# Kernel optimization log

Hardware: AMD Instinct MI355X
Metric: run time of the kernel (lower is better)

Reference implementation:

```python
import jax, jax.numpy as jnp
import numpy as np

B, H, O, T = 4096, 256, 128, 200

def setup_inputs() -> dict:
    key = jax.random.key(0)
    ks = jax.random.split(key, 8)
    s = 1.0 / np.sqrt(H)
    return {
        "C": jax.random.normal(ks[0], (B, H), dtype=jnp.float32),
        "t": jax.random.randint(ks[1], (B,), 0, T),
        "mask": jnp.ones((B, T), dtype=jnp.float32),
        "W_ih": jax.random.uniform(ks[2], (4 * H, H), jnp.float32, -s, s),
        "W_hh": jax.random.uniform(ks[3], (4 * H, H), jnp.float32, -s, s),
        "b_ih": jax.random.uniform(ks[4], (4 * H,), jnp.float32, -s, s),
        "b_hh": jax.random.uniform(ks[5], (4 * H,), jnp.float32, -s, s),
        "W_lin": jax.random.uniform(ks[6], (O, H), jnp.float32, -s, s),
        "b_lin": jax.random.uniform(ks[7], (O,), jnp.float32, -s, s),
    }

def reference(C, t, mask, W_ih, W_hh, b_ih, b_hh, W_lin, b_lin):
    # Input projection is constant across time (same C fed every step).
    x_proj = C @ W_ih.T + b_ih + b_hh  # [B, 4H]
    h0 = jnp.zeros((C.shape[0], W_hh.shape[1]), dtype=C.dtype)
    c0 = jnp.zeros_like(h0)

    def step(carry, _):
        h, c = carry
        gates = x_proj + h @ W_hh.T          # [B, 4H], torch gate order i,f,g,o
        i, f, g, o = jnp.split(gates, 4, axis=-1)
        i = jax.nn.sigmoid(i)
        f = jax.nn.sigmoid(f)
        g = jnp.tanh(g)
        o = jax.nn.sigmoid(o)
        c = f * c + i * g
        h = o * jnp.tanh(c)
        y = h @ W_lin.T + b_lin              # [B, O]
        return (h, c), y

    _, ys = jax.lax.scan(step, (h0, c0), xs=None, length=T)
    return ys  # [T, B, O]
```

## Files before the change

### kernel.cpp

```cpp
#include <hip/hip_runtime.h>


#define B_SZ 4096
#define H_SZ 256
#define O_SZ 128
#define T_SZ 200
#define SW   2032.0f
#define SG   (1.0f/(127.0f*2032.0f))

typedef __bf16 b16x8 __attribute__((ext_vector_type(8)));
typedef float f32x4 __attribute__((ext_vector_type(4)));
typedef int   i32x4 __attribute__((ext_vector_type(4)));
typedef unsigned short u16x8 __attribute__((ext_vector_type(8)));

typedef __attribute__((address_space(1))) const void gas_void;
typedef __attribute__((address_space(3))) void las_void;

__device__ __forceinline__ unsigned short f2bf(float x){
  unsigned u = __builtin_bit_cast(unsigned, x);
  u += 0x7FFFu + ((u >> 16) & 1u);
  return (unsigned short)(u >> 16);
}
__device__ __forceinline__ float bf2f(unsigned short h){
  unsigned u = ((unsigned)h) << 16;
  return __builtin_bit_cast(float, u);
}
__device__ __forceinline__ float fsig(float x){
  float t = __builtin_amdgcn_exp2f(-1.4426950408889634f * x);
  return __builtin_amdgcn_rcpf(1.0f + t);
}
__device__ __forceinline__ float ftanh(float x){
  x = fminf(fmaxf(x, -15.0f), 15.0f);
  float e = __builtin_amdgcn_exp2f(2.8853900817779268f * x);
  return (e - 1.0f) * __builtin_amdgcn_rcpf(e + 1.0f);
}
__device__ __forceinline__ f32x4 mfma16(b16x8 a, b16x8 b, f32x4 c){
  return __builtin_amdgcn_mfma_f32_16x16x32_bf16(a, b, c, 0, 0, 0);
}
__device__ __forceinline__ i32x4 mfma_i8(i32x4 a, i32x4 b, i32x4 c){
  return __builtin_amdgcn_mfma_i32_16x16x64_i8(a, b, c, 0, 0, 0);
}

__global__ void lstm_setup(const float* __restrict__ Wih, const float* __restrict__ Whh,
                           const float* __restrict__ Wlin, const float* __restrict__ bih,
                           const float* __restrict__ bhh, const float* __restrict__ C,
                           unsigned short* __restrict__ pWih, signed char* __restrict__ qWhh,
                           signed char* __restrict__ qWlin, float* __restrict__ bias,
                           unsigned short* __restrict__ Chi, unsigned short* __restrict__ Clo)
{
  const int nW  = 262144;
  const int nQ  = 262144;
  const int nL  = 32768;
  const int nB  = 1024;
  const int nC  = 1048576;
  long i = (long)blockIdx.x * blockDim.x + threadIdx.x;
  if (i < nW){
    int d = (int)i;
    int j = d & 7, l = (d >> 3) & 63, nt = (d >> 9) & 63, kk = (d >> 15) & 7;
    int src = (nt * 16 + (l & 15)) * H_SZ + kk * 32 + (l >> 4) * 8 + j;
    pWih[d] = f2bf(Wih[src]);
  } else if (i < nW + nQ){
    int d = (int)(i - nW);
    int j = d & 15, l = (d >> 4) & 63, kk = (d >> 10) & 3, nt = d >> 12;
    int n = nt * 16 + (l & 15), k = kk * 64 + (l >> 4) * 16 + j;
    qWhh[d] = (signed char)(int)rintf(Whh[n * H_SZ + k] * SW);
  } else if (i < nW + nQ + nL){
    int d = (int)(i - nW - nQ);
    int j = d & 15, l = (d >> 4) & 63, kk = (d >> 10) & 3, nt = d >> 12;
    int n = nt * 16 + (l & 15), k = kk * 64 + (l >> 4) * 16 + j;
    qWlin[d] = (signed char)(int)rintf(Wlin[n * H_SZ + k] * SW);
  } else if (i < nW + nQ + nL + nB){
    int d = (int)(i - nW - nQ - nL);
    bias[d] = bih[d] + bhh[d];
  } else if (i < nW + nQ + nL + nB + nC){
    int d = (int)(i - nW - nQ - nL - nB);
    float c = C[d];
    unsigned short hi = f2bf(c);
    Chi[d] = hi;
    Clo[d] = f2bf(c - bf2f(hi));
  }
}

__device__ __forceinline__ b16x8 ldsA(const unsigned short* hb, int row, int kbyte){
  int off = row * 512 + (kbyte ^ ((row & 15) << 4));
  return *(const b16x8*)((const char*)hb + off);
}
__device__ __forceinline__ b16x8 ldB2(const unsigned short* __restrict__ p, int ntile, int kk, int l){
  return *(const b16x8*)(p + (((kk * 64 + ntile) << 6) + l) * 8);
}
__device__ __forceinline__ i32x4 ldh(const char* h8, int row, int kbase){
  int off = row * 256 + (kbase ^ ((row & 15) << 4));
  return *(const i32x4*)(h8 + off);
}

__launch_bounds__(1024, 1)
__global__ void lstm_main(const unsigned short* __restrict__ pWih,
                          const signed char* __restrict__ qWhh,
                          const signed char* __restrict__ qWlin,
                          const float* __restrict__ bias,
                          const unsigned short* __restrict__ Chi,
                          const unsigned short* __restrict__ Clo,
                          const float* __restrict__ blin,
                          float* __restrict__ out)
{
  __shared__ char smem[4096 + 32768];
  char* h8 = smem;
  char* wlin = smem + 4096;
  unsigned short* ctile = (unsigned short*)(smem + 4096);

  const int tid = threadIdx.x;
  const int w = tid >> 6, l = tid & 63;
  const int lm = l & 15, lg = l >> 4;
  const int B0 = blockIdx.x * 16;

  f32x4 accf[4];
  const f32x4 zf = {0.f,0.f,0.f,0.f};
  #pragma unroll
  for (int g = 0; g < 4; g++) accf[g] = zf;

  for (int pass = 0; pass < 2; pass++){
    const unsigned short* Csrc = pass ? Clo : Chi;
    __syncthreads();
    if (tid < 512){
      int r = tid >> 5, c0 = (tid & 31) * 8;
      u16x8 v = *(const u16x8*)(Csrc + (long)(B0 + r) * H_SZ + c0);
      *(u16x8*)((char*)ctile + r * 512 + ((c0 * 2) ^ (r << 4))) = v;
    }
    __syncthreads();
    #pragma unroll
    for (int kk = 0; kk < 8; kk++){
      b16x8 a0 = ldsA(ctile, lm, kk * 64 + lg * 16);
      #pragma unroll
      for (int g = 0; g < 4; g++){
        b16x8 b = ldB2(pWih, g * 16 + w, kk, l);
        accf[g] = mfma16(a0, b, accf[g]);
      }
    }
  }
  f32x4 xpf[4];
  #pragma unroll
  for (int g = 0; g < 4; g++){
    float bv = bias[(g * 16 + w) * 16 + lm];
    #pragma unroll
    for (int r = 0; r < 4; r++) xpf[g][r] = accf[g][r] + bv;
  }
  __syncthreads();

  i32x4 bW[4][4];
  #pragma unroll
  for (int g = 0; g < 4; g++)
    #pragma unroll
    for (int kk = 0; kk < 4; kk++)
      bW[g][kk] = *(const i32x4*)(qWhh + ((g * 16 + w) * 4 + kk) * 1024 + l * 16);
  #pragma unroll
  for (int f = 0; f < 2; f++)
    __builtin_amdgcn_global_load_lds(
        (gas_void*)(qWlin + (w * 2 + f) * 1024 + l * 16),
        (las_void*)(wlin + (w * 2 + f) * 1024 + l * 16), 16, 0, 0);
  float bl = (w < 8) ? blin[w * 16 + lm] : 0.f;

  float cst[4];
  #pragma unroll
  for (int r = 0; r < 4; r++) cst[r] = 0.f;

  *(unsigned*)(h8 + tid * 4) = 0u;
  asm volatile("s_waitcnt vmcnt(0) lgkmcnt(0)" ::: "memory");
  __builtin_amdgcn_s_barrier();

  for (int t = 0; t < T_SZ; t++){
    i32x4 acci[4];
    const i32x4 zi = {0,0,0,0};
    #pragma unroll
    for (int g = 0; g < 4; g++) acci[g] = zi;

    #pragma unroll
    for (int kk = 0; kk < 4; kk++){
      i32x4 a = ldh(h8, lm, kk * 64 + lg * 16);
      #pragma unroll
      for (int g = 0; g < 4; g++)
        acci[g] = mfma_i8(a, bW[g][kk], acci[g]);
    }
    asm volatile("s_waitcnt lgkmcnt(0)" ::: "memory");
    __builtin_amdgcn_s_barrier();

    #pragma unroll
    for (int r = 0; r < 4; r++){
      float iv = fsig (SG * (float)acci[0][r] + xpf[0][r]);
      float fv = fsig (SG * (float)acci[1][r] + xpf[1][r]);
      float gv = ftanh(SG * (float)acci[2][r] + xpf[2][r]);
      float ov = fsig (SG * (float)acci[3][r] + xpf[3][r]);
      float cn = fv * cst[r] + iv * gv;
      cst[r] = cn;
      float hv = ov * ftanh(cn);
      int row = lg * 4 + r;
      int col = w * 16 + lm;
      h8[row * 256 + (col ^ (row << 4))] = (signed char)(int)rintf(hv * 127.0f);
    }
    asm volatile("s_waitcnt lgkmcnt(0)" ::: "memory");
    __builtin_amdgcn_s_barrier();

    if (w < 8){
      i32x4 ya = zi;
      #pragma unroll
      for (int kk = 0; kk < 4; kk++){
        i32x4 a  = ldh(h8, lm, kk * 64 + lg * 16);
        i32x4 bb = *(const i32x4*)(wlin + (w * 4 + kk) * 1024 + l * 16);
        ya = mfma_i8(a, bb, ya);
      }
      float* op = out + (long)t * (B_SZ * O_SZ) + (long)B0 * O_SZ;
      #pragma unroll
      for (int r = 0; r < 4; r++){
        int row = lg * 4 + r;
        __builtin_nontemporal_store(SG * (float)ya[r] + bl, op + row * O_SZ + w * 16 + lm);
      }
    }
  }
}

extern "C" void kernel_launch(void* const* d_in, const int* in_sizes, int n_in,
                              void* d_out, int out_size, void* d_ws, size_t ws_size,
                              hipStream_t stream)
{
  const float* C    = (const float*)d_in[0];
  const float* Wih  = (const float*)d_in[3];
  const float* Whh  = (const float*)d_in[4];
  const float* bih  = (const float*)d_in[5];
  const float* bhh  = (const float*)d_in[6];
  const float* Wlin = (const float*)d_in[7];
  const float* blin = (const float*)d_in[8];
  float* out = (float*)d_out;

  char* ws = (char*)d_ws;
  unsigned short* pWih = (unsigned short*)(ws);
  signed char*    qWhh = (signed char*)(ws + 524288);
  signed char*    qWlin= (signed char*)(ws + 786432);
  float*          bias = (float*)(ws + 819200);
  unsigned short* Chi  = (unsigned short*)(ws + 823296);
  unsigned short* Clo  = (unsigned short*)(ws + 2920448);

  int total = 262144 + 262144 + 32768 + 1024 + 1048576;
  lstm_setup<<<dim3((total + 255) / 256), dim3(256), 0, stream>>>(
      Wih, Whh, Wlin, bih, bhh, C, pWih, qWhh, qWlin, bias, Chi, Clo);
  lstm_main<<<dim3(256), dim3(1024), 0, stream>>>(
      pWih, qWhh, qWlin, bias, Chi, Clo, blin, out);
}
```

Before: 410.1 us.

## Double-buffer hidden state and defer output projection to drop a barrier

The int8 hidden state in LDS is double-buffered, so each step reads h from one buffer and writes the next into the other. This removes one of the two per-step barriers. The output projection for step t-1 now reuses the h fragments already loaded for the recurrent matmul, with a final epilogue for the last step. Gate nonlinearities are also folded so the exp2 scale constants are premultiplied into x_proj and the accumulator scale, and tanh is expressed via a sigmoid-style rcp. Costs are extra LDS and the loss of the tanh clamp, which could overflow exp2 for large arguments (rcp of inf gives 0, so the result stays finite).

```diff
diff --git a/kernel.cpp b/kernel.cpp
--- a/kernel.cpp
+++ b/kernel.cpp
@@ -7,6 +7,8 @@
 #define T_SZ 200
 #define SW   2032.0f
 #define SG   (1.0f/(127.0f*2032.0f))
+#define KC   (-1.4426950408889634f)
+#define K2C  (-2.8853900817779268f)
 
 typedef __bf16 b16x8 __attribute__((ext_vector_type(8)));
 typedef float f32x4 __attribute__((ext_vector_type(4)));
@@ -25,15 +27,8 @@
   unsigned u = ((unsigned)h) << 16;
   return __builtin_bit_cast(float, u);
 }
-__device__ __forceinline__ float fsig(float x){
-  float t = __builtin_amdgcn_exp2f(-1.4426950408889634f * x);
-  return __builtin_amdgcn_rcpf(1.0f + t);
-}
-__device__ __forceinline__ float ftanh(float x){
-  x = fminf(fmaxf(x, -15.0f), 15.0f);
-  float e = __builtin_amdgcn_exp2f(2.8853900817779268f * x);
-  return (e - 1.0f) * __builtin_amdgcn_rcpf(e + 1.0f);
-}
+__device__ __forceinline__ float fexp2(float x){ return __builtin_amdgcn_exp2f(x); }
+__device__ __forceinline__ float frcp(float x){ return __builtin_amdgcn_rcpf(x); }
 __device__ __forceinline__ f32x4 mfma16(b16x8 a, b16x8 b, f32x4 c){
   return __builtin_amdgcn_mfma_f32_16x16x32_bf16(a, b, c, 0, 0, 0);
 }
@@ -103,10 +98,10 @@
                           const float* __restrict__ blin,
                           float* __restrict__ out)
 {
-  __shared__ char smem[4096 + 32768];
+  __shared__ char smem[8192 + 32768];
   char* h8 = smem;
-  char* wlin = smem + 4096;
-  unsigned short* ctile = (unsigned short*)(smem + 4096);
+  char* wlin = smem + 8192;
+  unsigned short* ctile = (unsigned short*)(smem + 8192);
 
   const int tid = threadIdx.x;
   const int w = tid >> 6, l = tid & 63;
@@ -137,12 +132,13 @@
       }
     }
   }
-  f32x4 xpf[4];
+  f32x4 xs[4];
   #pragma unroll
   for (int g = 0; g < 4; g++){
     float bv = bias[(g * 16 + w) * 16 + lm];
-    #pragma unroll
-    for (int r = 0; r < 4; r++) xpf[g][r] = accf[g][r] + bv;
+    float sc = (g == 2) ? K2C : KC;
+    #pragma unroll
+    for (int r = 0; r < 4; r++) xs[g][r] = sc * (accf[g][r] + bv);
   }
   __syncthreads();
 
@@ -163,57 +159,84 @@
   #pragma unroll
   for (int r = 0; r < 4; r++) cst[r] = 0.f;
 
-  *(unsigned*)(h8 + tid * 4) = 0u;
+  *(unsigned long long*)(h8 + tid * 8) = 0ull;
   asm volatile("s_waitcnt vmcnt(0) lgkmcnt(0)" ::: "memory");
   __builtin_amdgcn_s_barrier();
 
+  const float KnS  = KC  * SG;
+  const float K2S  = K2C * SG;
+  const i32x4 zi = {0,0,0,0};
+
   for (int t = 0; t < T_SZ; t++){
+    const char* hrd = h8 + (t & 1) * 4096;
+    char*       hwr = h8 + ((t + 1) & 1) * 4096;
+
+    i32x4 a[4];
+    #pragma unroll
+    for (int kk = 0; kk < 4; kk++) a[kk] = ldh(hrd, lm, kk * 64 + lg * 16);
+
     i32x4 acci[4];
-    const i32x4 zi = {0,0,0,0};
     #pragma unroll
     for (int g = 0; g < 4; g++) acci[g] = zi;
-
-    #pragma unroll
-    for (int kk = 0; kk < 4; kk++){
-      i32x4 a = ldh(h8, lm, kk * 64 + lg * 16);
+    #pragma unroll
+    for (int kk = 0; kk < 4; kk++)
       #pragma unroll
       for (int g = 0; g < 4; g++)
-        acci[g] = mfma_i8(a, bW[g][kk], acci[g]);
-    }
-    asm volatile("s_waitcnt lgkmcnt(0)" ::: "memory");
-    __builtin_amdgcn_s_barrier();
-
-    #pragma unroll
-    for (int r = 0; r < 4; r++){
-      float iv = fsig (SG * (float)acci[0][r] + xpf[0][r]);
-      float fv = fsig (SG * (float)acci[1][r] + xpf[1][r]);
-      float gv = ftanh(SG * (float)acci[2][r] + xpf[2][r]);
-      float ov = fsig (SG * (float)acci[3][r] + xpf[3][r]);
-      float cn = fv * cst[r] + iv * gv;
-      cst[r] = cn;
-      float hv = ov * ftanh(cn);
-      int row = lg * 4 + r;
-      int col = w * 16 + lm;
-      h8[row * 256 + (col ^ (row << 4))] = (signed char)(int)rintf(hv * 127.0f);
-    }
-    asm volatile("s_waitcnt lgkmcnt(0)" ::: "memory");
-    __builtin_amdgcn_s_barrier();
+        acci[g] = mfma_i8(a[kk], bW[g][kk], acci[g]);
 
     if (w < 8){
       i32x4 ya = zi;
       #pragma unroll
       for (int kk = 0; kk < 4; kk++){
-        i32x4 a  = ldh(h8, lm, kk * 64 + lg * 16);
         i32x4 bb = *(const i32x4*)(wlin + (w * 4 + kk) * 1024 + l * 16);
-        ya = mfma_i8(a, bb, ya);
+        ya = mfma_i8(a[kk], bb, ya);
       }
-      float* op = out + (long)t * (B_SZ * O_SZ) + (long)B0 * O_SZ;
-      #pragma unroll
-      for (int r = 0; r < 4; r++){
-        int row = lg * 4 + r;
-        __builtin_nontemporal_store(SG * (float)ya[r] + bl, op + row * O_SZ + w * 16 + lm);
+      if (t > 0){
+        float* op = out + (long)(t - 1) * (B_SZ * O_SZ) + (long)B0 * O_SZ;
+        #pragma unroll
+        for (int r = 0; r < 4; r++)
+          __builtin_nontemporal_store(SG * (float)ya[r] + bl,
+                                      op + (lg * 4 + r) * O_SZ + w * 16 + lm);
       }
     }
+
+    #pragma unroll
+    for (int r = 0; r < 4; r++){
+      float ui = __builtin_fmaf(KnS, (float)acci[0][r], xs[0][r]);
+      float uf = __builtin_fmaf(KnS, (float)acci[1][r], xs[1][r]);
+      float ug = __builtin_fmaf(K2S, (float)acci[2][r], xs[2][r]);
+      float uo = __builtin_fmaf(KnS, (float)acci[3][r], xs[3][r]);
+      float iv = frcp(1.0f + fexp2(ui));
+      float fv = frcp(1.0f + fexp2(uf));
+      float rg = frcp(1.0f + fexp2(ug));
+      float ov = frcp(1.0f + fexp2(uo));
+      float gv = __builtin_fmaf(2.0f, rg, -1.0f);
+      float cn = __builtin_fmaf(fv, cst[r], iv * gv);
+      cst[r] = cn;
+      float rc = frcp(1.0f + fexp2(K2C * cn));
+      float hv = ov * __builtin_fmaf(2.0f, rc, -1.0f);
+      int row = lg * 4 + r;
+      int col = w * 16 + lm;
+      hwr[row * 256 + (col ^ (row << 4))] = (signed char)(int)rintf(hv * 127.0f);
+    }
+    asm volatile("s_waitcnt lgkmcnt(0)" ::: "memory");
+    __builtin_amdgcn_s_barrier();
+  }
+
+  if (w < 8){
+    const char* hrd = h8 + ((T_SZ) & 1) * 4096;
+    i32x4 ya = zi;
+    #pragma unroll
+    for (int kk = 0; kk < 4; kk++){
+      i32x4 a  = ldh(hrd, lm, kk * 64 + lg * 16);
+      i32x4 bb = *(const i32x4*)(wlin + (w * 4 + kk) * 1024 + l * 16);
+      ya = mfma_i8(a, bb, ya);
+    }
+    float* op = out + (long)(T_SZ - 1) * (B_SZ * O_SZ) + (long)B0 * O_SZ;
+    #pragma unroll
+    for (int r = 0; r < 4; r++)
+      __builtin_nontemporal_store(SG * (float)ya[r] + bl,
+                                  op + (lg * 4 + r) * O_SZ + w * 16 + lm);
   }
 }
 
```

Result: slower. 667.4 us (+62.7%).
